# Optimization experiments

Hardware: AMD Instinct MI355X
Metric: run time of the kernel (lower is better)

## Reference

```python
import jax, jax.numpy as jnp
import numpy as np

D_IN = 1024
D_OUT = 1024
N_HEADS = 16
HEAD_DIM = D_OUT // N_HEADS


def setup_inputs() -> dict:
    key = jax.random.key(0)
    ks = jax.random.split(key, 6)
    s = 0.02
    return {
        "X": jax.random.normal(ks[0], (4, 2048, D_IN), dtype=jnp.float32),
        "W_K": jax.random.normal(ks[1], (D_IN, D_OUT), dtype=jnp.float32) * s,
        "W_Q": jax.random.normal(ks[2], (D_IN, D_OUT), dtype=jnp.float32) * s,
        "W_V": jax.random.normal(ks[3], (D_IN, D_OUT), dtype=jnp.float32) * s,
        "W_out": jax.random.normal(ks[4], (D_OUT, D_OUT), dtype=jnp.float32) * s,
        "b_out": jax.random.normal(ks[5], (D_OUT,), dtype=jnp.float32) * s,
    }


def reference(X, W_K, W_Q, W_V, W_out, b_out):
    B, S, _ = X.shape
    # QKV projections (no bias, qkv_bias=False)
    Q = (X @ W_Q).reshape(B, S, N_HEADS, HEAD_DIM).transpose(0, 2, 1, 3)  # [B,H,S,Dh]
    K = (X @ W_K).reshape(B, S, N_HEADS, HEAD_DIM).transpose(0, 2, 1, 3)
    V = (X @ W_V).reshape(B, S, N_HEADS, HEAD_DIM).transpose(0, 2, 1, 3)
    # scores, causal mask, scale (mask-then-scale == scale-then-mask for -inf)
    scores = jnp.einsum("bhqd,bhkd->bhqk", Q, K) / jnp.sqrt(jnp.float32(HEAD_DIM))
    causal = jnp.tril(jnp.ones((S, S), dtype=bool))
    scores = jnp.where(causal, scores, -jnp.inf)
    W = jax.nn.softmax(scores, axis=-1)
    # dropout is identity in eval mode (deterministic reference)
    C = jnp.einsum("bhqk,bhkd->bhqd", W, V)  # [B,H,S,Dh]
    C = C.transpose(0, 2, 1, 3).reshape(B, S, D_OUT)
    return C @ W_out + b_out
```

## Files before the change

### kernel.cpp

```cpp
#include <hip/hip_runtime.h>

typedef float  f32x4  __attribute__((ext_vector_type(4)));
typedef float  f32x16 __attribute__((ext_vector_type(16)));
typedef __bf16 bf16x8 __attribute__((ext_vector_type(8)));
typedef unsigned int u32x4 __attribute__((ext_vector_type(4)));

#define DIM   1024
#define SEQ   2048
#define HDIM  64

static __device__ __forceinline__ unsigned short f2bf(float f) {
  unsigned int u = __builtin_bit_cast(unsigned int, f);
  u += 0x7fffu + ((u >> 16) & 1u);
  return (unsigned short)(u >> 16);
}

static __device__ __forceinline__ float exp2a(float x) {
#if __has_builtin(__builtin_amdgcn_exp2f)
  return __builtin_amdgcn_exp2f(x);
#else
  return exp2f(x);
#endif
}

static __device__ __forceinline__ void pswap(unsigned& a, unsigned& b) {
#if __has_builtin(__builtin_amdgcn_permlane32_swap)
  auto r = __builtin_amdgcn_permlane32_swap(a, b, false, false);
  a = r[0]; b = r[1];
#else
  asm volatile("v_permlane32_swap_b32 %0, %1" : "+v"(a), "+v"(b));
#endif
}

#define CVTPK(lo_, hi_) ({ unsigned r_;                                                 \
  asm("v_cvt_pk_bf16_f32 %0, %1, %2" : "=v"(r_) : "v"(lo_), "v"(hi_)); r_; })

#define GLDS16(g, l)                                                                    \
  __builtin_amdgcn_global_load_lds((__attribute__((address_space(1))) void*)(g),        \
                                   (__attribute__((address_space(3))) void*)(l), 16, 0, 0)

__global__ __launch_bounds__(256) void convert_x(const float4* __restrict__ X,
                                                 ushort4* __restrict__ Xb) {
  int i = blockIdx.x * 256 + threadIdx.x;
  float4 v = X[i];
  ushort4 o;
  o.x = f2bf(v.x); o.y = f2bf(v.y); o.z = f2bf(v.z); o.w = f2bf(v.w);
  Xb[i] = o;
}

__global__ __launch_bounds__(256) void transpose_w(const float* __restrict__ WQ,
                                                   const float* __restrict__ WK,
                                                   const float* __restrict__ WV,
                                                   const float* __restrict__ WO,
                                                   unsigned short* __restrict__ WtAll) {
  const int z = blockIdx.z;
  const float* W = (z == 0) ? WQ : (z == 1) ? WK : (z == 2) ? WV : WO;
  unsigned short* Wt = WtAll + (size_t)z * (DIM * DIM);
  __shared__ float tile[32][33];
  const int tx = threadIdx.x, ty = threadIdx.y;
  const int n0 = blockIdx.x * 32, k0 = blockIdx.y * 32;
#pragma unroll
  for (int r = 0; r < 4; ++r)
    tile[ty + 8 * r][tx] = W[(size_t)(k0 + ty + 8 * r) * DIM + n0 + tx];
  __syncthreads();
#pragma unroll
  for (int r = 0; r < 4; ++r)
    Wt[(size_t)(n0 + ty + 8 * r) * DIM + k0 + tx] = f2bf(tile[tx][ty + 8 * r]);
}

__global__ __launch_bounds__(256) void gemm_qkv(const unsigned short* __restrict__ Xb,
                                                const unsigned short* __restrict__ WtAll,
                                                unsigned short* __restrict__ Qb,
                                                unsigned short* __restrict__ Kh,
                                                unsigned short* __restrict__ Vb) {
  const int z = blockIdx.z;
  const unsigned short* Wt = WtAll + (size_t)z * (DIM * DIM);
  const int m0 = blockIdx.x * 128, n0 = blockIdx.y * 128;
  const int lane = threadIdx.x & 63, wave = threadIdx.x >> 6;
  const int wr = wave >> 1, wc = wave & 1;
  const int l15 = lane & 15, lg = lane >> 4;
  const int rowA = lane >> 2;
  const int colS = (((lane & 3) ^ ((rowA >> 1) & 3)) * 8);
  const int slotS = ((lg ^ ((l15 >> 1) & 3)) * 8);
  const int sA = wave * 2;
  __shared__ __align__(16) unsigned short As[2][128 * 32], Bs[2][128 * 32];
  f32x4 acc[4][4] = {};

  auto STAGE = [&](int buf, int kt) {
    GLDS16(Xb + (size_t)(m0 + (sA + 0) * 16 + rowA) * DIM + kt + colS, &As[buf][(sA + 0) * 512]);
    GLDS16(Xb + (size_t)(m0 + (sA + 1) * 16 + rowA) * DIM + kt + colS, &As[buf][(sA + 1) * 512]);
    GLDS16(Wt + (size_t)(n0 + (sA + 0) * 16 + rowA) * DIM + kt + colS, &Bs[buf][(sA + 0) * 512]);
    GLDS16(Wt + (size_t)(n0 + (sA + 1) * 16 + rowA) * DIM + kt + colS, &Bs[buf][(sA + 1) * 512]);
  };

  STAGE(0, 0);
  __syncthreads();
  int cur = 0;
  for (int kt = 0; kt < DIM; kt += 32) {
    if (kt + 32 < DIM) STAGE(cur ^ 1, kt + 32);
    bf16x8 af[4], bfr[4];
#pragma unroll
    for (int mi = 0; mi < 4; ++mi)
      af[mi] = *(const bf16x8*)&As[cur][(wr * 64 + mi * 16 + l15) * 32 + slotS];
#pragma unroll
    for (int ni = 0; ni < 4; ++ni)
      bfr[ni] = *(const bf16x8*)&Bs[cur][(wc * 64 + ni * 16 + l15) * 32 + slotS];
    if (z < 2) {
#pragma unroll
      for (int mi = 0; mi < 4; ++mi)
#pragma unroll
        for (int ni = 0; ni < 4; ++ni)
          acc[mi][ni] = __builtin_amdgcn_mfma_f32_16x16x32_bf16(bfr[ni], af[mi], acc[mi][ni], 0, 0, 0);
    } else {
#pragma unroll
      for (int mi = 0; mi < 4; ++mi)
#pragma unroll
        for (int ni = 0; ni < 4; ++ni)
          acc[mi][ni] = __builtin_amdgcn_mfma_f32_16x16x32_bf16(af[mi], bfr[ni], acc[mi][ni], 0, 0, 0);
    }
    __syncthreads();
    cur ^= 1;
  }

  if (z == 0) {
    const float scale = (float)(0.125 * 1.4426950408889634);
#pragma unroll
    for (int mi = 0; mi < 4; ++mi)
#pragma unroll
      for (int ni = 0; ni < 4; ++ni) {
        const int s = m0 + wr * 64 + mi * 16 + l15;
        const int nb = n0 + wc * 64 + ni * 16 + lg * 4;
        ushort4 v;
        v.x = f2bf(acc[mi][ni][0] * scale); v.y = f2bf(acc[mi][ni][1] * scale);
        v.z = f2bf(acc[mi][ni][2] * scale); v.w = f2bf(acc[mi][ni][3] * scale);
        *(ushort4*)&Qb[(size_t)s * DIM + nb] = v;
      }
  } else if (z == 1) {
#pragma unroll
    for (int mi = 0; mi < 4; ++mi)
#pragma unroll
      for (int ni = 0; ni < 4; ++ni) {
        const int s = m0 + wr * 64 + mi * 16 + l15;
        const int b = s >> 11, sl = s & 2047;
        const int nb = n0 + wc * 64 + ni * 16 + lg * 4;
        const int h = nb >> 6, d = nb & 63;
        ushort4 v;
        v.x = f2bf(acc[mi][ni][0]); v.y = f2bf(acc[mi][ni][1]);
        v.z = f2bf(acc[mi][ni][2]); v.w = f2bf(acc[mi][ni][3]);
        *(ushort4*)&Kh[((size_t)(b * 16 + h) * 2048 + sl) * 64 + d] = v;
      }
  } else {
#pragma unroll
    for (int mi = 0; mi < 4; ++mi)
#pragma unroll
      for (int ni = 0; ni < 4; ++ni) {
        const int n = n0 + wc * 64 + ni * 16 + l15;
        const int h = n >> 6, d = n & 63;
        const int mb = m0 + wr * 64 + mi * 16 + lg * 4;
        const int b = mb >> 11, s = mb & 2047;
        const int t = s >> 6, si = s & 63;
        ushort4 v;
        v.x = f2bf(acc[mi][ni][0]); v.y = f2bf(acc[mi][ni][1]);
        v.z = f2bf(acc[mi][ni][2]); v.w = f2bf(acc[mi][ni][3]);
        *(ushort4*)&Vb[((((size_t)(b * 16 + h) * 32 + t) * 64 + d) * 64) + si] = v;
      }
  }
}

__global__ __launch_bounds__(256) void attn(const unsigned short* __restrict__ Qb,
                                            const unsigned short* __restrict__ Kh,
                                            const unsigned short* __restrict__ Vb,
                                            unsigned short* __restrict__ Cb) {
  const int bh = blockIdx.x;
  const int qt = (gridDim.y - 1) - blockIdx.y;
  const int b = bh >> 4;
  const int tid = threadIdx.x;
  const int lane = tid & 63, wave = tid >> 6;
  const int l31 = lane & 31, hi = lane >> 5;
  const int swz = (l31 & 7) << 4;
  const int q_base = qt * 128 + wave * 32;
  const int q = q_base + l31;

  __shared__ __align__(16) char LDS[2][16384];

  int soff0, soff1;
  {
    const int L0 = wave * 2048 + lane * 16;
    const int r0 = L0 >> 7;
    soff0 = r0 * 128 + ((L0 & 127) ^ ((r0 & 7) << 4));
    const int L1 = L0 + 1024;
    const int r1 = L1 >> 7;
    soff1 = r1 * 128 + ((L1 & 127) ^ ((r1 & 7) << 4));
  }
  const char* Kt0 = (const char*)Kh + ((size_t)bh * 2048) * 128;
  const char* Vt0 = (const char*)Vb + ((size_t)bh * 32) * 8192;

  const unsigned short* Qp = Qb + (size_t)(b * SEQ + q) * DIM + (bh & 15) * HDIM + hi * 8;
  bf16x8 qf[4];
#pragma unroll
  for (int ks = 0; ks < 4; ++ks) qf[ks] = *(const bf16x8*)(Qp + ks * 16);

  float m_r = -INFINITY, l_r = 0.f;
  f32x16 o0 = {}, o1 = {};

  const int n_tiles = 2 * qt + 2;
  int cur = 0;

  {
    char* lK = &LDS[0][wave * 2048];
    char* lV = &LDS[0][8192 + wave * 2048];
    GLDS16(Kt0 + soff0, lK); GLDS16(Kt0 + soff1, lK + 1024);
    GLDS16(Vt0 + soff0, lV); GLDS16(Vt0 + soff1, lV + 1024);
  }
  __syncthreads();

  for (int t = 0; t < n_tiles; ++t) {
    const int kv0 = t << 6;
    if (t + 1 < n_tiles) {
      const char* kb = Kt0 + (size_t)(t + 1) * 8192;
      const char* vb = Vt0 + (size_t)(t + 1) * 8192;
      char* lK = &LDS[cur ^ 1][wave * 2048];
      char* lV = &LDS[cur ^ 1][8192 + wave * 2048];
      GLDS16(kb + soff0, lK); GLDS16(kb + soff1, lK + 1024);
      GLDS16(vb + soff0, lV); GLDS16(vb + soff1, lV + 1024);
    }

    if (kv0 <= q_base + 31) {
      const char* Lb = &LDS[cur][0];
      f32x16 st0 = {}, st1 = {};
      __builtin_amdgcn_s_setprio(1);
#pragma unroll
      for (int ks = 0; ks < 4; ++ks) {
        const char* a = Lb + l31 * 128 + ((ks * 32 + hi * 16) ^ swz);
        bf16x8 kf0 = *(const bf16x8*)(a);
        bf16x8 kf1 = *(const bf16x8*)(a + 4096);
        st0 = __builtin_amdgcn_mfma_f32_32x32x16_bf16(kf0, qf[ks], st0, 0, 0, 0);
        st1 = __builtin_amdgcn_mfma_f32_32x32x16_bf16(kf1, qf[ks], st1, 0, 0, 0);
      }
      __builtin_amdgcn_s_setprio(0);

      if (kv0 + 63 > q_base) {
        const int qm = q - kv0 - 4 * hi;
#pragma unroll
        for (int r = 0; r < 16; ++r) {
          const int c = (r & 3) + 8 * (r >> 2);
          if (c > qm)      st0[r] = -INFINITY;
          if (c + 32 > qm) st1[r] = -INFINITY;
        }
      }

      float tmax = st0[0];
#pragma unroll
      for (int r = 1; r < 16; ++r) tmax = fmaxf(tmax, st0[r]);
#pragma unroll
      for (int r = 0; r < 16; ++r) tmax = fmaxf(tmax, st1[r]);
      tmax = fmaxf(tmax, __shfl_xor(tmax, 32));

      if (__any(!(tmax <= m_r + 8.0f))) {
        const float mn = fmaxf(m_r, tmax);
        const float al = exp2a(m_r - mn);
        m_r = mn;
        l_r *= al;
        o0 *= al;
        o1 *= al;
      }

#pragma unroll
      for (int r = 0; r < 16; ++r) st0[r] = exp2a(st0[r] - m_r);
#pragma unroll
      for (int r = 0; r < 16; ++r) st1[r] = exp2a(st1[r] - m_r);
      float ps = 0.f;
#pragma unroll
      for (int r = 0; r < 16; ++r) ps += st0[r] + st1[r];
      ps += __shfl_xor(ps, 32);
      l_r += ps;

      u32x4 pf[4];
      {
        unsigned a, bb;
        a = CVTPK(st0[0], st0[1]);   bb = CVTPK(st0[4], st0[5]);   pswap(a, bb); pf[0][0] = a; pf[0][2] = bb;
        a = CVTPK(st0[2], st0[3]);   bb = CVTPK(st0[6], st0[7]);   pswap(a, bb); pf[0][1] = a; pf[0][3] = bb;
        a = CVTPK(st0[8], st0[9]);   bb = CVTPK(st0[12], st0[13]); pswap(a, bb); pf[1][0] = a; pf[1][2] = bb;
        a = CVTPK(st0[10], st0[11]); bb = CVTPK(st0[14], st0[15]); pswap(a, bb); pf[1][1] = a; pf[1][3] = bb;
        a = CVTPK(st1[0], st1[1]);   bb = CVTPK(st1[4], st1[5]);   pswap(a, bb); pf[2][0] = a; pf[2][2] = bb;
        a = CVTPK(st1[2], st1[3]);   bb = CVTPK(st1[6], st1[7]);   pswap(a, bb); pf[2][1] = a; pf[2][3] = bb;
        a = CVTPK(st1[8], st1[9]);   bb = CVTPK(st1[12], st1[13]); pswap(a, bb); pf[3][0] = a; pf[3][2] = bb;
        a = CVTPK(st1[10], st1[11]); bb = CVTPK(st1[14], st1[15]); pswap(a, bb); pf[3][1] = a; pf[3][3] = bb;
      }

      __builtin_amdgcn_s_setprio(1);
#pragma unroll
      for (int ks = 0; ks < 4; ++ks) {
        const char* a = Lb + 8192 + l31 * 128 + ((ks * 32 + hi * 16) ^ swz);
        bf16x8 v0 = *(const bf16x8*)(a);
        bf16x8 v1 = *(const bf16x8*)(a + 4096);
        bf16x8 pb = __builtin_bit_cast(bf16x8, pf[ks]);
        o0 = __builtin_amdgcn_mfma_f32_32x32x16_bf16(v0, pb, o0, 0, 0, 0);
        o1 = __builtin_amdgcn_mfma_f32_32x32x16_bf16(v1, pb, o1, 0, 0, 0);
      }
      __builtin_amdgcn_s_setprio(0);
    }

    __syncthreads();
    cur ^= 1;
  }

  const float rl = 1.0f / l_r;
  unsigned short* Co = Cb + (size_t)(b * SEQ + q) * DIM + (bh & 15) * HDIM;
#pragma unroll
  for (int j = 0; j < 4; ++j) {
    ushort4 w0, w1;
    w0.x = f2bf(o0[4 * j + 0] * rl); w0.y = f2bf(o0[4 * j + 1] * rl);
    w0.z = f2bf(o0[4 * j + 2] * rl); w0.w = f2bf(o0[4 * j + 3] * rl);
    w1.x = f2bf(o1[4 * j + 0] * rl); w1.y = f2bf(o1[4 * j + 1] * rl);
    w1.z = f2bf(o1[4 * j + 2] * rl); w1.w = f2bf(o1[4 * j + 3] * rl);
    *(ushort4*)(Co + 8 * j + 4 * hi) = w0;
    *(ushort4*)(Co + 32 + 8 * j + 4 * hi) = w1;
  }
}

__global__ __launch_bounds__(256) void gemm_out(const unsigned short* __restrict__ Cb,
                                                const unsigned short* __restrict__ WtO,
                                                const float* __restrict__ bias,
                                                float* __restrict__ out) {
  const int m0 = blockIdx.x * 128, n0 = blockIdx.y * 128;
  const int lane = threadIdx.x & 63, wave = threadIdx.x >> 6;
  const int wr = wave >> 1, wc = wave & 1;
  const int l15 = lane & 15, lg = lane >> 4;
  const int rowA = lane >> 2;
  const int colS = (((lane & 3) ^ ((rowA >> 1) & 3)) * 8);
  const int slotS = ((lg ^ ((l15 >> 1) & 3)) * 8);
  const int sA = wave * 2;
  __shared__ __align__(16) unsigned short As[2][128 * 32], Bs[2][128 * 32];
  f32x4 acc[4][4] = {};

  auto STAGE = [&](int buf, int kt) {
    GLDS16(Cb  + (size_t)(m0 + (sA + 0) * 16 + rowA) * DIM + kt + colS, &As[buf][(sA + 0) * 512]);
    GLDS16(Cb  + (size_t)(m0 + (sA + 1) * 16 + rowA) * DIM + kt + colS, &As[buf][(sA + 1) * 512]);
    GLDS16(WtO + (size_t)(n0 + (sA + 0) * 16 + rowA) * DIM + kt + colS, &Bs[buf][(sA + 0) * 512]);
    GLDS16(WtO + (size_t)(n0 + (sA + 1) * 16 + rowA) * DIM + kt + colS, &Bs[buf][(sA + 1) * 512]);
  };

  STAGE(0, 0);
  __syncthreads();
  int cur = 0;
  for (int kt = 0; kt < DIM; kt += 32) {
    if (kt + 32 < DIM) STAGE(cur ^ 1, kt + 32);
    bf16x8 af[4], bfr[4];
#pragma unroll
    for (int mi = 0; mi < 4; ++mi)
      af[mi] = *(const bf16x8*)&As[cur][(wr * 64 + mi * 16 + l15) * 32 + slotS];
#pragma unroll
    for (int ni = 0; ni < 4; ++ni)
      bfr[ni] = *(const bf16x8*)&Bs[cur][(wc * 64 + ni * 16 + l15) * 32 + slotS];
#pragma unroll
    for (int mi = 0; mi < 4; ++mi)
#pragma unroll
      for (int ni = 0; ni < 4; ++ni)
        acc[mi][ni] = __builtin_amdgcn_mfma_f32_16x16x32_bf16(bfr[ni], af[mi], acc[mi][ni], 0, 0, 0);
    __syncthreads();
    cur ^= 1;
  }

#pragma unroll
  for (int mi = 0; mi < 4; ++mi)
#pragma unroll
    for (int ni = 0; ni < 4; ++ni) {
      const int s = m0 + wr * 64 + mi * 16 + l15;
      const int nb = n0 + wc * 64 + ni * 16 + lg * 4;
      const float4 bv = *(const float4*)&bias[nb];
      float4 o;
      o.x = acc[mi][ni][0] + bv.x; o.y = acc[mi][ni][1] + bv.y;
      o.z = acc[mi][ni][2] + bv.z; o.w = acc[mi][ni][3] + bv.w;
      *(float4*)&out[(size_t)s * DIM + nb] = o;
    }
}

extern "C" void kernel_launch(void* const* d_in, const int* in_sizes, int n_in,
                              void* d_out, int out_size, void* d_ws, size_t ws_size,
                              hipStream_t stream) {
  const float* X  = (const float*)d_in[0];
  const float* WK = (const float*)d_in[1];
  const float* WQ = (const float*)d_in[2];
  const float* WV = (const float*)d_in[3];
  const float* WO = (const float*)d_in[4];
  const float* bo = (const float*)d_in[5];
  float* out = (float*)d_out;

  char* ws = (char*)d_ws;
  unsigned short* Xb    = (unsigned short*)(ws);
  unsigned short* WtAll = (unsigned short*)(ws + (16u << 20));
  unsigned short* Qb    = (unsigned short*)(ws + (24u << 20));
  unsigned short* Kh    = (unsigned short*)(ws + (40u << 20));
  unsigned short* Vb    = (unsigned short*)(ws + (56u << 20));
  unsigned short* Cb    = Xb;

  convert_x<<<8192, 256, 0, stream>>>((const float4*)X, (ushort4*)Xb);
  transpose_w<<<dim3(32, 32, 4), dim3(32, 8), 0, stream>>>(WQ, WK, WV, WO, WtAll);
  gemm_qkv<<<dim3(64, 8, 3), 256, 0, stream>>>(Xb, WtAll, Qb, Kh, Vb);
  attn<<<dim3(64, 16), 256, 0, stream>>>(Qb, Kh, Vb, Cb);
  gemm_out<<<dim3(64, 8), 256, 0, stream>>>(Cb, WtAll + 3u * 1048576u, bo, out);
}
```

Baseline: 262.0 us.

## Rewrite QKV GEMM with 256x128 tiles, triple-buffered LDS pipeline, and fused prep kernel

The QKV projection GEMM is restructured into a 512-thread kernel with 256x128 output tiles and a K step of 64. It adds a three-stage global-to-LDS pipeline with split issue, XOR-swizzled LDS addressing, setprio around the MFMA bursts and a workgroup index swizzle for cache locality. The X conversion and weight transpose are merged into one launch to save a kernel launch. These changes aim to raise MFMA utilisation and hide memory latency, at the cost of more LDS use and delicate vmcnt bookkeeping.

```diff
diff --git a/kernel.cpp b/kernel.cpp
--- a/kernel.cpp
+++ b/kernel.cpp
@@ -39,88 +39,145 @@
   __builtin_amdgcn_global_load_lds((__attribute__((address_space(1))) void*)(g),        \
                                    (__attribute__((address_space(3))) void*)(l), 16, 0, 0)
 
-__global__ __launch_bounds__(256) void convert_x(const float4* __restrict__ X,
-                                                 ushort4* __restrict__ Xb) {
-  int i = blockIdx.x * 256 + threadIdx.x;
-  float4 v = X[i];
-  ushort4 o;
-  o.x = f2bf(v.x); o.y = f2bf(v.y); o.z = f2bf(v.z); o.w = f2bf(v.w);
-  Xb[i] = o;
-}
-
-__global__ __launch_bounds__(256) void transpose_w(const float* __restrict__ WQ,
-                                                   const float* __restrict__ WK,
-                                                   const float* __restrict__ WV,
-                                                   const float* __restrict__ WO,
-                                                   unsigned short* __restrict__ WtAll) {
-  const int z = blockIdx.z;
-  const float* W = (z == 0) ? WQ : (z == 1) ? WK : (z == 2) ? WV : WO;
-  unsigned short* Wt = WtAll + (size_t)z * (DIM * DIM);
+__global__ __launch_bounds__(256) void prep(const float* __restrict__ X,
+                                            ushort4* __restrict__ Xb,
+                                            const float* __restrict__ WQ,
+                                            const float* __restrict__ WK,
+                                            const float* __restrict__ WV,
+                                            const float* __restrict__ WO,
+                                            unsigned short* __restrict__ WtAll) {
+  const int bid = blockIdx.x;
   __shared__ float tile[32][33];
-  const int tx = threadIdx.x, ty = threadIdx.y;
-  const int n0 = blockIdx.x * 32, k0 = blockIdx.y * 32;
-#pragma unroll
-  for (int r = 0; r < 4; ++r)
-    tile[ty + 8 * r][tx] = W[(size_t)(k0 + ty + 8 * r) * DIM + n0 + tx];
-  __syncthreads();
-#pragma unroll
-  for (int r = 0; r < 4; ++r)
-    Wt[(size_t)(n0 + ty + 8 * r) * DIM + k0 + tx] = f2bf(tile[tx][ty + 8 * r]);
-}
-
-__global__ __launch_bounds__(256) void gemm_qkv(const unsigned short* __restrict__ Xb,
-                                                const unsigned short* __restrict__ WtAll,
-                                                unsigned short* __restrict__ Qb,
-                                                unsigned short* __restrict__ Kh,
-                                                unsigned short* __restrict__ Vb) {
-  const int z = blockIdx.z;
-  const unsigned short* Wt = WtAll + (size_t)z * (DIM * DIM);
-  const int m0 = blockIdx.x * 128, n0 = blockIdx.y * 128;
+  if (bid < 8192) {
+    int i = bid * 256 + threadIdx.x;
+    float4 v = ((const float4*)X)[i];
+    ushort4 o;
+    o.x = f2bf(v.x); o.y = f2bf(v.y); o.z = f2bf(v.z); o.w = f2bf(v.w);
+    Xb[i] = o;
+  } else {
+    const int b2 = bid - 8192;
+    const int z = b2 >> 10;
+    const int xy = b2 & 1023;
+    const int bx = xy & 31, by = xy >> 5;
+    const float* W = (z == 0) ? WQ : (z == 1) ? WK : (z == 2) ? WV : WO;
+    unsigned short* Wt = WtAll + (size_t)z * (DIM * DIM);
+    const int tx = threadIdx.x & 31, ty = threadIdx.x >> 5;
+    const int n0 = bx * 32, k0 = by * 32;
+#pragma unroll
+    for (int r = 0; r < 4; ++r)
+      tile[ty + 8 * r][tx] = W[(size_t)(k0 + ty + 8 * r) * DIM + n0 + tx];
+    __syncthreads();
+#pragma unroll
+    for (int r = 0; r < 4; ++r)
+      Wt[(size_t)(n0 + ty + 8 * r) * DIM + k0 + tx] = f2bf(tile[tx][ty + 8 * r]);
+  }
+}
+
+template<bool SW>
+static __device__ __forceinline__ void kloop8(const unsigned short* __restrict__ Xb,
+                                              const unsigned short* __restrict__ Wt3,
+                                              unsigned short* As, unsigned short* Bs,
+                                              int m0, int n0g, f32x4 acc[4][4]) {
+  const int tid = threadIdx.x;
+  const int lane = tid & 63, wave = tid >> 6;
+  const int l15 = lane & 15, lg = lane >> 4;
+  const int wm = (wave >> 1) * 64, wn = (wave & 1) * 64;
+  const int rswz = (l15 & 7) << 4;
+
+  const int rA = tid >> 3;
+  const int cx = ((tid & 7) * 16) ^ ((rA & 7) << 4);
+  const char* gA = (const char*)Xb + ((size_t)(m0 + rA) * DIM) * 2 + cx;
+  const char* gB = (const char*)Wt3 + ((size_t)(n0g + rA) * DIM) * 2 + cx;
+
+  auto STAGE_A = [&](int buf, int kt, int j) {
+    GLDS16(gA + (size_t)j * (64 * 2048) + kt * 2, &As[buf * 16384 + j * 4096 + wave * 512]);
+  };
+  auto STAGE_B = [&](int buf, int kt, int j) {
+    GLDS16(gB + (size_t)j * (64 * 2048) + kt * 2, &Bs[buf * 8192 + j * 4096 + wave * 512]);
+  };
+  auto LDA = [&](int buf, int fr, int kk) {
+    return *(const bf16x8*)&As[buf * 16384 + (wm + fr * 16 + l15) * 64 +
+                               (((kk * 64 + lg * 16) ^ rswz) >> 1)];
+  };
+  auto LDB = [&](int buf, int ni, int kk) {
+    return *(const bf16x8*)&Bs[buf * 8192 + (wn + ni * 16 + l15) * 64 +
+                               (((kk * 64 + lg * 16) ^ rswz) >> 1)];
+  };
+
+#pragma unroll
+  for (int j = 0; j < 4; ++j) STAGE_A(0, 0, j);
+#pragma unroll
+  for (int j = 0; j < 2; ++j) STAGE_B(0, 0, j);
+#pragma unroll
+  for (int j = 0; j < 4; ++j) STAGE_A(1, 64, j);
+#pragma unroll
+  for (int j = 0; j < 2; ++j) STAGE_B(1, 64, j);
+  asm volatile("s_waitcnt vmcnt(6)" ::: "memory");
+  __builtin_amdgcn_s_barrier();
+
+  for (int t = 0; t < 16; ++t) {
+    const int buf = t % 3;
+    const int b2 = (t + 2) % 3;
+    const int kt2 = (t + 2) * 64;
+    const bool pre = (t + 2) < 16;
+    bf16x8 bq[4][2];
+#pragma unroll
+    for (int p = 0; p < 4; ++p) {
+      if (pre) {
+        if (p == 0) { STAGE_A(b2, kt2, 0); STAGE_A(b2, kt2, 1); STAGE_A(b2, kt2, 2); }
+        else if (p == 1) { STAGE_A(b2, kt2, 3); STAGE_B(b2, kt2, 0); STAGE_B(b2, kt2, 1); }
+      }
+      if (p == 0) {
+#pragma unroll
+        for (int ni = 0; ni < 4; ++ni) {
+          bq[ni][0] = LDB(buf, ni, 0);
+          bq[ni][1] = LDB(buf, ni, 1);
+        }
+      }
+      bf16x8 a0 = LDA(buf, p, 0);
+      bf16x8 a1 = LDA(buf, p, 1);
+      asm volatile("s_waitcnt lgkmcnt(0)" ::: "memory");
+      __builtin_amdgcn_sched_barrier(0);
+      __builtin_amdgcn_s_setprio(1);
+#pragma unroll
+      for (int ni = 0; ni < 4; ++ni) {
+        if (SW) {
+          acc[p][ni] = __builtin_amdgcn_mfma_f32_16x16x32_bf16(bq[ni][0], a0, acc[p][ni], 0, 0, 0);
+          acc[p][ni] = __builtin_amdgcn_mfma_f32_16x16x32_bf16(bq[ni][1], a1, acc[p][ni], 0, 0, 0);
+        } else {
+          acc[p][ni] = __builtin_amdgcn_mfma_f32_16x16x32_bf16(a0, bq[ni][0], acc[p][ni], 0, 0, 0);
+          acc[p][ni] = __builtin_amdgcn_mfma_f32_16x16x32_bf16(a1, bq[ni][1], acc[p][ni], 0, 0, 0);
+        }
+      }
+      __builtin_amdgcn_s_setprio(0);
+      if (p < 3) __builtin_amdgcn_s_barrier();
+    }
+    if (t < 14)       asm volatile("s_waitcnt vmcnt(6)" ::: "memory");
+    else if (t == 14) asm volatile("s_waitcnt vmcnt(0)" ::: "memory");
+    __builtin_amdgcn_s_barrier();
+  }
+}
+
+__global__ __launch_bounds__(512) void gemm_qkv8(const unsigned short* __restrict__ Xb,
+                                                 const unsigned short* __restrict__ WtAll,
+                                                 unsigned short* __restrict__ Qb,
+                                                 unsigned short* __restrict__ Kh,
+                                                 unsigned short* __restrict__ Vb) {
+  __shared__ __align__(16) unsigned short As[3 * 16384];
+  __shared__ __align__(16) unsigned short Bs[3 * 8192];
+  const int wg = blockIdx.x;
+  const int sw = (wg & 7) * 96 + (wg >> 3);
+  const int ntile = sw >> 5, mtile = sw & 31;
+  const int m0 = mtile * 256, n0g = ntile * 128;
+  const int z = n0g >> 10, n0z = n0g & 1023;
+
+  f32x4 acc[4][4] = {};
+  if (z < 2) kloop8<true>(Xb, WtAll, As, Bs, m0, n0g, acc);
+  else       kloop8<false>(Xb, WtAll, As, Bs, m0, n0g, acc);
+
   const int lane = threadIdx.x & 63, wave = threadIdx.x >> 6;
-  const int wr = wave >> 1, wc = wave & 1;
   const int l15 = lane & 15, lg = lane >> 4;
-  const int rowA = lane >> 2;
-  const int colS = (((lane & 3) ^ ((rowA >> 1) & 3)) * 8);
-  const int slotS = ((lg ^ ((l15 >> 1) & 3)) * 8);
-  const int sA = wave * 2;
-  __shared__ __align__(16) unsigned short As[2][128 * 32], Bs[2][128 * 32];
-  f32x4 acc[4][4] = {};
-
-  auto STAGE = [&](int buf, int kt) {
-    GLDS16(Xb + (size_t)(m0 + (sA + 0) * 16 + rowA) * DIM + kt + colS, &As[buf][(sA + 0) * 512]);
-    GLDS16(Xb + (size_t)(m0 + (sA + 1) * 16 + rowA) * DIM + kt + colS, &As[buf][(sA + 1) * 512]);
-    GLDS16(Wt + (size_t)(n0 + (sA + 0) * 16 + rowA) * DIM + kt + colS, &Bs[buf][(sA + 0) * 512]);
-    GLDS16(Wt + (size_t)(n0 + (sA + 1) * 16 + rowA) * DIM + kt + colS, &Bs[buf][(sA + 1) * 512]);
-  };
-
-  STAGE(0, 0);
-  __syncthreads();
-  int cur = 0;
-  for (int kt = 0; kt < DIM; kt += 32) {
-    if (kt + 32 < DIM) STAGE(cur ^ 1, kt + 32);
-    bf16x8 af[4], bfr[4];
-#pragma unroll
-    for (int mi = 0; mi < 4; ++mi)
-      af[mi] = *(const bf16x8*)&As[cur][(wr * 64 + mi * 16 + l15) * 32 + slotS];
-#pragma unroll
-    for (int ni = 0; ni < 4; ++ni)
-      bfr[ni] = *(const bf16x8*)&Bs[cur][(wc * 64 + ni * 16 + l15) * 32 + slotS];
-    if (z < 2) {
-#pragma unroll
-      for (int mi = 0; mi < 4; ++mi)
-#pragma unroll
-        for (int ni = 0; ni < 4; ++ni)
-          acc[mi][ni] = __builtin_amdgcn_mfma_f32_16x16x32_bf16(bfr[ni], af[mi], acc[mi][ni], 0, 0, 0);
-    } else {
-#pragma unroll
-      for (int mi = 0; mi < 4; ++mi)
-#pragma unroll
-        for (int ni = 0; ni < 4; ++ni)
-          acc[mi][ni] = __builtin_amdgcn_mfma_f32_16x16x32_bf16(af[mi], bfr[ni], acc[mi][ni], 0, 0, 0);
-    }
-    __syncthreads();
-    cur ^= 1;
-  }
+  const int wm = (wave >> 1) * 64, wn = (wave & 1) * 64;
 
   if (z == 0) {
     const float scale = (float)(0.125 * 1.4426950408889634);
@@ -128,22 +185,22 @@
     for (int mi = 0; mi < 4; ++mi)
 #pragma unroll
       for (int ni = 0; ni < 4; ++ni) {
-        const int s = m0 + wr * 64 + mi * 16 + l15;
-        const int nb = n0 + wc * 64 + ni * 16 + lg * 4;
+        const int s = m0 + wm + mi * 16 + l15;
+        const int nq = n0z + wn + ni * 16 + lg * 4;
         ushort4 v;
         v.x = f2bf(acc[mi][ni][0] * scale); v.y = f2bf(acc[mi][ni][1] * scale);
         v.z = f2bf(acc[mi][ni][2] * scale); v.w = f2bf(acc[mi][ni][3] * scale);
-        *(ushort4*)&Qb[(size_t)s * DIM + nb] = v;
+        *(ushort4*)&Qb[(size_t)s * DIM + nq] = v;
       }
   } else if (z == 1) {
 #pragma unroll
     for (int mi = 0; mi < 4; ++mi)
 #pragma unroll
       for (int ni = 0; ni < 4; ++ni) {
-        const int s = m0 + wr * 64 + mi * 16 + l15;
+        const int s = m0 + wm + mi * 16 + l15;
         const int b = s >> 11, sl = s & 2047;
-        const int nb = n0 + wc * 64 + ni * 16 + lg * 4;
-        const int h = nb >> 6, d = nb & 63;
+        const int nq = n0z + wn + ni * 16 + lg * 4;
+        const int h = nq >> 6, d = nq & 63;
         ushort4 v;
         v.x = f2bf(acc[mi][ni][0]); v.y = f2bf(acc[mi][ni][1]);
         v.z = f2bf(acc[mi][ni][2]); v.w = f2bf(acc[mi][ni][3]);
@@ -154,15 +211,15 @@
     for (int mi = 0; mi < 4; ++mi)
 #pragma unroll
       for (int ni = 0; ni < 4; ++ni) {
-        const int n = n0 + wc * 64 + ni * 16 + l15;
+        const int n = n0z + wn + ni * 16 + l15;
         const int h = n >> 6, d = n & 63;
-        const int mb = m0 + wr * 64 + mi * 16 + lg * 4;
-        const int b = mb >> 11, s = mb & 2047;
-        const int t = s >> 6, si = s & 63;
+        const int s4 = m0 + wm + mi * 16 + lg * 4;
+        const int b = s4 >> 11, sq = s4 & 2047;
+        const int tt = sq >> 6, si = sq & 63;
         ushort4 v;
         v.x = f2bf(acc[mi][ni][0]); v.y = f2bf(acc[mi][ni][1]);
         v.z = f2bf(acc[mi][ni][2]); v.w = f2bf(acc[mi][ni][3]);
-        *(ushort4*)&Vb[((((size_t)(b * 16 + h) * 32 + t) * 64 + d) * 64) + si] = v;
+        *(ushort4*)&Vb[((((size_t)(b * 16 + h) * 32 + tt) * 64 + d) * 64) + si] = v;
       }
   }
 }
@@ -395,9 +452,8 @@
   unsigned short* Vb    = (unsigned short*)(ws + (56u << 20));
   unsigned short* Cb    = Xb;
 
-  convert_x<<<8192, 256, 0, stream>>>((const float4*)X, (ushort4*)Xb);
-  transpose_w<<<dim3(32, 32, 4), dim3(32, 8), 0, stream>>>(WQ, WK, WV, WO, WtAll);
-  gemm_qkv<<<dim3(64, 8, 3), 256, 0, stream>>>(Xb, WtAll, Qb, Kh, Vb);
+  prep<<<12288, 256, 0, stream>>>(X, (ushort4*)Xb, WQ, WK, WV, WO, WtAll);
+  gemm_qkv8<<<768, 512, 0, stream>>>(Xb, WtAll, Qb, Kh, Vb);
   attn<<<dim3(64, 16), 256, 0, stream>>>(Qb, Kh, Vb, Cb);
   gemm_out<<<dim3(64, 8), 256, 0, stream>>>(Cb, WtAll + 3u * 1048576u, bo, out);
 }
```

Measured after the change: 288.5 us. +10.1%, slower.
